# Kernel optimization log

Hardware: AMD Instinct MI355X
Metric: run time of the kernel (lower is better)

## Reference

```python
import jax, jax.numpy as jnp
import numpy as np

B, T, D, S = 32, 4096, 64, 64
H = 128  # emission MLP hidden width
EPS = 1e-10
NEG = 1e10


def setup_inputs() -> dict:
    key = jax.random.key(0)
    ks = jax.random.split(key, 8)

    def dense_init(k, shape):
        return jax.random.normal(k, shape, jnp.float32) / jnp.sqrt(shape[0])

    return {
        "observations": jax.random.normal(ks[0], (B, T, D), jnp.float32),
        "W1": dense_init(ks[1], (D, H)), "b1": jnp.zeros((H,), jnp.float32),
        "W2": dense_init(ks[2], (H, H)), "b2": jnp.zeros((H,), jnp.float32),
        "W3": dense_init(ks[3], (H, S)), "b3": jnp.zeros((S,), jnp.float32),
        "log_trans_matrix": jax.random.normal(ks[4], (S, S), jnp.float32) * 0.1,
        "log_init_probs": jnp.zeros((S,), jnp.float32),
        "log_r": jnp.ones((S,), jnp.float32),
        "logit_p": jnp.zeros((S,), jnp.float32),
    }


def reference(observations, W1, b1, W2, b2, W3, b3,
              log_trans_matrix, log_init_probs, log_r, logit_p):
    # ---- emission MLP + softmax ----  (B,T,D) -> (B,T,S)
    h = jax.nn.relu(observations @ W1 + b1)
    h = jax.nn.relu(h @ W2 + b2)
    emission_probs = jax.nn.softmax(h @ W3 + b3, axis=-1)
    log_em = jnp.log(emission_probs + EPS)  # (B,T,S)

    # ---- transition probs: self-transition masked softmax (S,S) ----
    eye = jnp.eye(S, dtype=jnp.float32)
    masked_logits = log_trans_matrix * (1.0 - eye) - NEG * eye
    trans_probs = jax.nn.softmax(masked_logits, axis=-1)  # (S,S)
    log_trans = jnp.log(trans_probs + EPS)

    # ---- forward recursion (scan over time) ----
    # NOTE: t=0 uses log(emission) WITHOUT eps, matching the torch source.
    la0 = jax.nn.log_softmax(log_init_probs) + jnp.log(emission_probs[:, 0])  # (B,S)

    def fstep(la, le_t):  # la:(B,S), le_t:(B,S)
        la_t = jax.nn.logsumexp(la[:, :, None] + log_trans[None], axis=1) + le_t
        return la_t, la_t

    le_rest = jnp.swapaxes(log_em[:, 1:], 0, 1)  # (T-1,B,S)
    _, las = jax.lax.scan(fstep, la0, le_rest)
    log_alpha = jnp.concatenate([la0[:, None], jnp.swapaxes(las, 0, 1)], axis=1)  # (B,T,S)

    # ---- backward recursion ----
    lbT = jnp.zeros((B, S), jnp.float32)

    def bstep(lb, le_t1):  # combine emission(t+1)+beta(t+1) over next-state axis
        lb_t = jax.nn.logsumexp(log_trans[None] + (le_t1 + lb)[:, None, :], axis=2)
        return lb_t, lb_t

    _, lbs = jax.lax.scan(bstep, lbT, le_rest[::-1])  # lbs[0] is t=T-2
    log_beta = jnp.concatenate(
        [jnp.swapaxes(lbs, 0, 1)[:, ::-1], lbT[:, None]], axis=1)  # (B,T,S)

    # ---- posteriors ----
    log_gamma = log_alpha + log_beta
    log_gamma = log_gamma - jax.nn.logsumexp(log_gamma, axis=-1, keepdims=True)
    state_probs = jnp.exp(log_gamma)  # (B,T,S)
    state_marginals = state_probs.mean(axis=1)  # (B,S)

    # ---- expected durations (negative binomial) for all states ----
    r = jnp.exp(log_r)
    p = jax.nn.sigmoid(logit_p)
    expected_durations = r * (1.0 - p) / p  # (S,)

    # log-likelihood from final forward messages
    log_likelihood = jax.nn.logsumexp(log_alpha[:, -1], axis=-1)  # (B,)

    return state_probs, state_marginals, expected_durations, log_likelihood
```

## Files before the change

kernel.cpp:

```cpp
#include <hip/hip_runtime.h>

#define B_ 32
#define T_ 4096
#define D_ 64
#define H_ 128
#define S_ 64
#define BTS (B_*T_*S_)

#define NCH 256
#define CL  16
#define WU  16

#define EM_OFF    0
#define ALPHA_OFF (BTS/2)
#define BETA_OFF  BTS
#define P_OFF     (2*BTS)
#define PT_OFF    (2*BTS + 4096)
#define INITP_OFF (2*BTS + 8192)
#define WSPLIT_OFF (2*BTS - 32768)
#define SP_OFF   0
#define MARG_OFF BTS
#define DUR_OFF  (BTS + 2048)
#define LL_OFF   (BTS + 2112)

typedef __attribute__((ext_vector_type(8))) short short8;
typedef __attribute__((ext_vector_type(4))) short short4v;
typedef __attribute__((ext_vector_type(4))) float f32x4;
#define MFMA_BF16 __builtin_amdgcn_mfma_f32_16x16x32_bf16

__device__ __forceinline__ float wsum(float v) {
    #pragma unroll
    for (int m = 1; m < 64; m <<= 1) v += __shfl_xor(v, m, 64);
    return v;
}
__device__ __forceinline__ float wmax(float v) {
    #pragma unroll
    for (int m = 1; m < 64; m <<= 1) v = fmaxf(v, __shfl_xor(v, m, 64));
    return v;
}
__device__ __forceinline__ unsigned short bfhi(float x) {
    return (unsigned short)(__float_as_uint(x) >> 16);
}
__device__ __forceinline__ float bf2f(unsigned short h) {
    return __uint_as_float(((unsigned int)h) << 16);
}
__device__ __forceinline__ short8 cvt8(const float* x8) {
    int hv[4];
    #pragma unroll
    for (int p = 0; p < 4; p++) {
        int h;
        asm("v_cvt_pk_bf16_f32 %0, %1, %2" : "=v"(h) : "v"(x8[2*p]), "v"(x8[2*p+1]));
        hv[p] = h;
    }
    return *(short8*)hv;
}
__device__ __forceinline__ unsigned short bf16r(float x) {
    int h;
    asm("v_cvt_pk_bf16_f32 %0, %1, %2" : "=v"(h) : "v"(x), "v"(x));
    return (unsigned short)h;
}

__global__ __launch_bounds__(256) void prep_k(const float* __restrict__ LT,
                                              const float* __restrict__ lip,
                                              const float* __restrict__ logr,
                                              const float* __restrict__ logitp,
                                              const float* __restrict__ W1,
                                              const float* __restrict__ W2,
                                              const float* __restrict__ W3,
                                              float* __restrict__ ws,
                                              float* __restrict__ out) {
    int tid = threadIdx.x, wid = tid >> 6, lane = tid & 63;
    if (blockIdx.x == 0) {
        for (int r = wid; r < S_; r += 4) {
            float x = (lane == r) ? -1e10f : LT[r * S_ + lane];
            float m = wmax(x);
            float e = __expf(x - m);
            float s = wsum(e);
            float p = e / s + 1e-10f;
            ws[P_OFF  + r * S_ + lane] = p;
            ws[PT_OFF + lane * S_ + r] = p;
        }
        if (wid == 0) {
            float x = lip[lane];
            float m = wmax(x);
            float e = __expf(x - m);
            float s = wsum(e);
            ws[INITP_OFF + lane] = e / s;
        } else if (wid == 1) {
            float r = __expf(logr[lane]);
            float p = 1.f / (1.f + __expf(-logitp[lane]));
            out[DUR_OFF + lane] = r * (1.f - p) / p;
        }
        for (int i = tid; i < B_ * S_; i += 256) out[MARG_OFF + i] = 0.f;
        if (tid < B_) out[LL_OFF + tid] = 0.f;
    }
    int gid = blockIdx.x * 256 + tid, gstr = gridDim.x * 256;
    unsigned short* wsp = (unsigned short*)(ws + WSPLIT_OFF);
    for (int i = gid; i < 8192; i += gstr) {
        int j = i >> 6, d = i & 63;
        wsp[i] = bfhi(W1[d * 128 + j]);
    }
    for (int i = gid; i < 16384; i += gstr) {
        int j = i >> 7, k = i & 127;
        wsp[16384 + i] = bfhi(W2[k * 128 + j]);
    }
    for (int i = gid; i < 8192; i += gstr) {
        int s = i >> 7, k = i & 127;
        wsp[49152 + i] = bfhi(W3[k * 64 + s]);
    }
}

__global__ __launch_bounds__(256) void mlp_k(const float* __restrict__ obs,
                                             const unsigned short* __restrict__ wsp,
                                             const float* __restrict__ b1,
                                             const float* __restrict__ b2,
                                             const float* __restrict__ b3,
                                             unsigned short* __restrict__ em) {
    __shared__ unsigned short hl[4 * 2 * 2176];
    int tid = threadIdx.x, wid = tid >> 6, lane = tid & 63;
    int c = lane & 15, q = lane >> 4;
    unsigned short* hb = hl + wid * 4352;
    int r0 = blockIdx.x * 128 + wid * 32;

    short8 a1[2][2];
    #pragma unroll
    for (int mt = 0; mt < 2; mt++) {
        #pragma unroll
        for (int kq = 0; kq < 2; kq++) {
            const float* xp = obs + (size_t)(r0 + mt * 16 + c) * 64 + kq * 32 + q * 8;
            float x8[8];
            *(float4*)x8       = *(const float4*)xp;
            *(float4*)(x8 + 4) = *(const float4*)(xp + 4);
            a1[mt][kq] = cvt8(x8);
        }
    }

    #pragma unroll
    for (int nt = 0; nt < 8; nt++) {
        const unsigned short* wp = wsp + (nt * 16 + c) * 64 + q * 8;
        short8 bh0 = *(const short8*)(wp);
        short8 bh1 = *(const short8*)(wp + 32);
        float bb = b1[nt * 16 + c];
        #pragma unroll
        for (int mt = 0; mt < 2; mt++) {
            f32x4 acc = {0.f, 0.f, 0.f, 0.f};
            acc = MFMA_BF16(a1[mt][0], bh0, acc, 0, 0, 0);
            acc = MFMA_BF16(a1[mt][1], bh1, acc, 0, 0, 0);
            #pragma unroll
            for (int r = 0; r < 4; r++)
                hb[mt * 2176 + (q * 4 + r) * 136 + nt * 16 + c] =
                    bf16r(fmaxf(acc[r] + bb, 0.f));
        }
    }

    short8 a2[2][4];
    #pragma unroll
    for (int mt = 0; mt < 2; mt++)
        #pragma unroll
        for (int kq = 0; kq < 4; kq++)
            a2[mt][kq] = *(const short8*)&hb[mt * 2176 + c * 136 + kq * 32 + q * 8];
    __asm__ __volatile__("s_waitcnt lgkmcnt(0)" ::: "memory");

    #pragma unroll
    for (int nt = 0; nt < 8; nt++) {
        const unsigned short* wp = wsp + 16384 + (nt * 16 + c) * 128 + q * 8;
        short8 bh[4];
        #pragma unroll
        for (int kq = 0; kq < 4; kq++)
            bh[kq] = *(const short8*)(wp + kq * 32);
        float bb = b2[nt * 16 + c];
        #pragma unroll
        for (int mt = 0; mt < 2; mt++) {
            f32x4 acc = {0.f, 0.f, 0.f, 0.f};
            #pragma unroll
            for (int kq = 0; kq < 4; kq++)
                acc = MFMA_BF16(a2[mt][kq], bh[kq], acc, 0, 0, 0);
            #pragma unroll
            for (int r = 0; r < 4; r++)
                hb[mt * 2176 + (q * 4 + r) * 136 + nt * 16 + c] =
                    bf16r(fmaxf(acc[r] + bb, 0.f));
        }
    }

    short8 a3[2][4];
    #pragma unroll
    for (int mt = 0; mt < 2; mt++)
        #pragma unroll
        for (int kq = 0; kq < 4; kq++)
            a3[mt][kq] = *(const short8*)&hb[mt * 2176 + c * 136 + kq * 32 + q * 8];
    __asm__ __volatile__("s_waitcnt lgkmcnt(0)" ::: "memory");

    f32x4 L[2][4];
    #pragma unroll
    for (int nt = 0; nt < 4; nt++) {
        const unsigned short* wp = wsp + 49152 + (nt * 16 + c) * 128 + q * 8;
        short8 bh[4];
        #pragma unroll
        for (int kq = 0; kq < 4; kq++)
            bh[kq] = *(const short8*)(wp + kq * 32);
        #pragma unroll
        for (int mt = 0; mt < 2; mt++) {
            f32x4 acc = {0.f, 0.f, 0.f, 0.f};
            #pragma unroll
            for (int kq = 0; kq < 4; kq++)
                acc = MFMA_BF16(a3[mt][kq], bh[kq], acc, 0, 0, 0);
            L[mt][nt] = acc;
        }
    }

    float bb3[4];
    #pragma unroll
    for (int nt = 0; nt < 4; nt++) bb3[nt] = b3[nt * 16 + c];
    #pragma unroll
    for (int mt = 0; mt < 2; mt++) {
        #pragma unroll
        for (int r = 0; r < 4; r++) {
            float v[4];
            #pragma unroll
            for (int nt = 0; nt < 4; nt++) v[nt] = L[mt][nt][r] + bb3[nt];
            float m = fmaxf(fmaxf(v[0], v[1]), fmaxf(v[2], v[3]));
            #pragma unroll
            for (int msk = 1; msk < 16; msk <<= 1) m = fmaxf(m, __shfl_xor(m, msk, 64));
            float e[4], s = 0.f;
            #pragma unroll
            for (int nt = 0; nt < 4; nt++) { e[nt] = __expf(v[nt] - m); s += e[nt]; }
            #pragma unroll
            for (int msk = 1; msk < 16; msk <<= 1) s += __shfl_xor(s, msk, 64);
            float rs = __builtin_amdgcn_rcpf(s);
            size_t row = (size_t)(r0 + mt * 16 + q * 4 + r);
            #pragma unroll
            for (int nt = 0; nt < 4; nt++)
                em[row * 64 + nt * 16 + c] = bf16r(e[nt] * rs);
        }
    }
}

__global__ __launch_bounds__(64) void scan_k(const unsigned short* __restrict__ em,
                                             const float* __restrict__ Pm,
                                             const float* __restrict__ PTm,
                                             const float* __restrict__ initp,
                                             unsigned short* __restrict__ alpha,
                                             unsigned short* __restrict__ beta,
                                             float* __restrict__ ll) {
    __shared__ float lds[16 * 68];
    const int lane = threadIdx.x, c = lane & 15, q = lane >> 4;
    int blk = blockIdx.x;
    const bool isf = blk < 2 * NCH;
    int lin = isf ? blk : blk - 2 * NCH;
    int bg = lin / NCH, ch = lin % NCH;
    const int b = bg * 16 + c;
    const float* M = isf ? PTm : Pm;

    short8 Bh[4][2];
    #pragma unroll
    for (int nt = 0; nt < 4; nt++) {
        #pragma unroll
        for (int kf = 0; kf < 2; kf++) {
            const float* mp = M + (nt * 16 + c) * 64 + kf * 32 + q * 8;
            float m8[8];
            *(float4*)m8       = *(const float4*)mp;
            *(float4*)(m8 + 4) = *(const float4*)(mp + 4);
            Bh[nt][kf] = cvt8(m8);
        }
    }

    const size_t ebase = (size_t)b * T_ * 64 + q * 8;
    unsigned short* outp = isf ? alpha : beta;
    const int wrofs = (q * 4) * 68 + c;
    const int rdofs = c * 68 + q * 8;

    float w[16];
    float rcpS, C = 0.f;

    auto loadE = [&](int t, float* e) {
        const unsigned short* p = em + ebase + (size_t)t * 64;
        short8 u0 = *(const short8*)(p);
        short8 u1 = *(const short8*)(p + 32);
        #pragma unroll
        for (int i = 0; i < 8; i++) {
            e[i]     = bf2f((unsigned short)u0[i]);
            e[8 + i] = bf2f((unsigned short)u1[i]);
        }
    };
    auto storeY = [&](const float* y, int t) {
        unsigned short* p = outp + ebase + (size_t)t * 64;
        *(short8*)(p)      = cvt8(y);
        *(short8*)(p + 32) = cvt8(y + 8);
    };
    auto chainsum = [&](const float* y) {
        float s = ((y[0]+y[1])+(y[2]+y[3])) + ((y[4]+y[5])+(y[6]+y[7]))
                + ((y[8]+y[9])+(y[10]+y[11])) + ((y[12]+y[13])+(y[14]+y[15]));
        s += __shfl_xor(s, 16, 64);
        s += __shfl_xor(s, 32, 64);
        return s;
    };
    auto matstep = [&](const float* z, float* y) {
        short8 ah0 = cvt8(z);
        short8 ah1 = cvt8(z + 8);
        f32x4 Dv[4];
        #pragma unroll
        for (int nt = 0; nt < 4; nt++) {
            f32x4 acc = {0.f, 0.f, 0.f, 0.f};
            acc = MFMA_BF16(ah0, Bh[nt][0], acc, 0, 0, 0);
            acc = MFMA_BF16(ah1, Bh[nt][1], acc, 0, 0, 0);
            Dv[nt] = acc;
        }
        #pragma unroll
        for (int r = 0; r < 4; r++) {
            lds[wrofs + r * 68]      = Dv[0][r];
            lds[wrofs + r * 68 + 16] = Dv[1][r];
            lds[wrofs + r * 68 + 32] = Dv[2][r];
            lds[wrofs + r * 68 + 48] = Dv[3][r];
        }
        __asm__ __volatile__("s_waitcnt lgkmcnt(0)" ::: "memory");
        *(float4*)(y)      = *(const float4*)&lds[rdofs];
        *(float4*)(y + 4)  = *(const float4*)&lds[rdofs + 4];
        *(float4*)(y + 8)  = *(const float4*)&lds[rdofs + 32];
        *(float4*)(y + 12) = *(const float4*)&lds[rdofs + 36];
        __asm__ __volatile__("s_waitcnt lgkmcnt(0)" ::: "memory");
    };

    if (isf) {
        const int wlo = ch * CL, te = wlo + CL - 1;
        int ts, nwarm;
        if (ch == 0) {
            float e[16], ip[16];
            loadE(0, e);
            const float* pp = initp + q * 8;
            *(float4*)(ip)      = *(const float4*)(pp);
            *(float4*)(ip + 4)  = *(const float4*)(pp + 4);
            *(float4*)(ip + 8)  = *(const float4*)(pp + 32);
            *(float4*)(ip + 12) = *(const float4*)(pp + 36);
            #pragma unroll
            for (int i = 0; i < 16; i++) w[i] = ip[i] * e[i];
            storeY(w, 0);
            float s = chainsum(w);
            rcpS = __builtin_amdgcn_rcpf(s);
            C = __log2f(s);
            ts = 1; nwarm = 0;
        } else {
            ts = wlo - WU; if (ts < 1) ts = 1;
            nwarm = wlo - ts;
            float e[16];
            loadE(ts - 1, e);
            #pragma unroll
            for (int i = 0; i < 16; i++) w[i] = e[i] + 1e-10f;
            float s = chainsum(w);
            rcpS = __builtin_amdgcn_rcpf(s);
            C = 0.f;
        }
        auto stepF = [&](int t, bool owned) {
            float e[16];
            loadE(t, e);
            float y[16];
            matstep(w, y);
            float epsr = 1e-10f * rcpS;
            #pragma unroll
            for (int i = 0; i < 16; i++) y[i] *= fmaf(e[i], rcpS, epsr);
            float s = chainsum(y);
            if (owned) { C += __log2f(s); storeY(y, t); }
            rcpS = __builtin_amdgcn_rcpf(s);
            #pragma unroll
            for (int i = 0; i < 16; i++) w[i] = y[i];
        };
        for (int i = 0; i < nwarm; i++) stepF(ts + i, false);
        for (int t = wlo > 0 ? wlo : 1; t <= te; t++) stepF(t, true);
        if (q == 0) atomicAdd(&ll[b], C * 0.69314718056f);
    } else {
        const int tlo = ch * CL;
        const int whi = (ch == NCH - 1) ? T_ - 2 : tlo + CL - 1;
        int ts, nwarm;
        if (ch == NCH - 1) {
            float ones[16];
            #pragma unroll
            for (int i = 0; i < 16; i++) ones[i] = 1.f;
            storeY(ones, T_ - 1);
            float e[16];
            loadE(T_ - 1, e);
            #pragma unroll
            for (int i = 0; i < 16; i++) w[i] = e[i] + 1e-10f;
            rcpS = 1.f / 64.f;
            nwarm = 0; ts = T_ - 2;
        } else {
            ts = whi + WU; if (ts > T_ - 2) ts = T_ - 2;
            nwarm = ts - whi;
            float e[16];
            loadE(ts + 1, e);
            #pragma unroll
            for (int i = 0; i < 16; i++) w[i] = e[i] + 1e-10f;
            rcpS = 1.f / 64.f;
        }
        auto stepB = [&](int t, bool owned) {
            float e[16];
            loadE(t, e);
            float y[16];
            matstep(w, y);
            #pragma unroll
            for (int i = 0; i < 16; i++) y[i] *= rcpS;
            float s = chainsum(y);
            if (owned) storeY(y, t);
            rcpS = __builtin_amdgcn_rcpf(s);
            #pragma unroll
            for (int i = 0; i < 16; i++) w[i] = y[i] * (e[i] + 1e-10f);
        };
        for (int i = 0; i < nwarm; i++) stepB(ts - i, false);
        for (int t = whi; t >= tlo; t--) stepB(t, true);
    }
}

__global__ __launch_bounds__(256) void gamma_k(const unsigned short* __restrict__ a16,
                                               const unsigned short* __restrict__ b16,
                                               float* __restrict__ out) {
    int tid = threadIdx.x;
    int wid = tid >> 6, lane = tid & 63;
    int c = lane & 15, q = lane >> 4;
    int b = blockIdx.x >> 5;
    int tile = blockIdx.x & 31;
    int t0 = tile * 128 + wid * 32;
    float m0 = 0.f, m1 = 0.f, m2 = 0.f, m3 = 0.f;
    #pragma unroll
    for (int it = 0; it < 8; it++) {
        int row = t0 + it * 4 + q;
        size_t off = ((size_t)b * T_ + row) * 64 + c * 4;
        short4v av = *(const short4v*)&a16[off];
        short4v bv = *(const short4v*)&b16[off];
        float px = bf2f((unsigned short)av[0]) * bf2f((unsigned short)bv[0]);
        float py = bf2f((unsigned short)av[1]) * bf2f((unsigned short)bv[1]);
        float pz = bf2f((unsigned short)av[2]) * bf2f((unsigned short)bv[2]);
        float pw = bf2f((unsigned short)av[3]) * bf2f((unsigned short)bv[3]);
        float s = (px + py) + (pz + pw);
        s += __shfl_xor(s, 1, 64);
        s += __shfl_xor(s, 2, 64);
        s += __shfl_xor(s, 4, 64);
        s += __shfl_xor(s, 8, 64);
        float rs = __builtin_amdgcn_rcpf(fmaxf(s, 1e-37f));
        float4 g;
        g.x = px * rs; g.y = py * rs; g.z = pz * rs; g.w = pw * rs;
        *(float4*)&out[SP_OFF + off] = g;
        m0 += g.x; m1 += g.y; m2 += g.z; m3 += g.w;
    }
    m0 += __shfl_xor(m0, 16, 64); m0 += __shfl_xor(m0, 32, 64);
    m1 += __shfl_xor(m1, 16, 64); m1 += __shfl_xor(m1, 32, 64);
    m2 += __shfl_xor(m2, 16, 64); m2 += __shfl_xor(m2, 32, 64);
    m3 += __shfl_xor(m3, 16, 64); m3 += __shfl_xor(m3, 32, 64);
    if (q == 0) {
        const float sc = 1.0f / T_;
        atomicAdd(&out[MARG_OFF + b * 64 + 4 * c + 0], m0 * sc);
        atomicAdd(&out[MARG_OFF + b * 64 + 4 * c + 1], m1 * sc);
        atomicAdd(&out[MARG_OFF + b * 64 + 4 * c + 2], m2 * sc);
        atomicAdd(&out[MARG_OFF + b * 64 + 4 * c + 3], m3 * sc);
    }
}

extern "C" void kernel_launch(void* const* d_in, const int* in_sizes, int n_in,
                              void* d_out, int out_size, void* d_ws, size_t ws_size,
                              hipStream_t stream) {
    (void)in_sizes; (void)n_in; (void)out_size; (void)ws_size;
    const float* obs    = (const float*)d_in[0];
    const float* W1     = (const float*)d_in[1];
    const float* b1     = (const float*)d_in[2];
    const float* W2     = (const float*)d_in[3];
    const float* b2     = (const float*)d_in[4];
    const float* W3     = (const float*)d_in[5];
    const float* b3     = (const float*)d_in[6];
    const float* LT     = (const float*)d_in[7];
    const float* lip    = (const float*)d_in[8];
    const float* logr   = (const float*)d_in[9];
    const float* logitp = (const float*)d_in[10];
    float* out = (float*)d_out;
    float* ws  = (float*)d_ws;

    unsigned short* em16 = (unsigned short*)(ws + EM_OFF);
    unsigned short* al16 = (unsigned short*)(ws + ALPHA_OFF);
    unsigned short* be16 = (unsigned short*)(ws + BETA_OFF);

    hipLaunchKernelGGL(prep_k, dim3(64), dim3(256), 0, stream,
                       LT, lip, logr, logitp, W1, W2, W3, ws, out);
    hipLaunchKernelGGL(mlp_k, dim3(1024), dim3(256), 0, stream,
                       obs, (const unsigned short*)(ws + WSPLIT_OFF),
                       b1, b2, b3, em16);
    hipLaunchKernelGGL(scan_k, dim3(4 * NCH), dim3(64), 0, stream,
                       em16, ws + P_OFF, ws + PT_OFF, ws + INITP_OFF,
                       al16, be16, out + LL_OFF);
    hipLaunchKernelGGL(gamma_k, dim3(1024), dim3(256), 0, stream,
                       al16, be16, out);
}
```

Measured before the change: 200.4 us.

## Prefetch next MLP weight tile during MFMAs and reduce WU to 12

The three emission MLP layers now software-pipeline their weight loads. The next column tile of weights is loaded into registers while the MFMAs for the current tile run, so global/L2 load latency is hidden behind compute. Separately, the WU constant (a warm-up length in the chunked recursion) drops from 16 to 12, which cuts redundant work in the scan but may affect accuracy at chunk boundaries. The prefetch raises register pressure.

```diff
diff --git a/kernel.cpp b/kernel.cpp
--- a/kernel.cpp
+++ b/kernel.cpp
@@ -9,7 +9,7 @@
 
 #define NCH 256
 #define CL  16
-#define WU  16
+#define WU  12
 
 #define EM_OFF    0
 #define ALPHA_OFF (BTS/2)
@@ -135,21 +135,29 @@
         }
     }
 
-    #pragma unroll
-    for (int nt = 0; nt < 8; nt++) {
-        const unsigned short* wp = wsp + (nt * 16 + c) * 64 + q * 8;
-        short8 bh0 = *(const short8*)(wp);
-        short8 bh1 = *(const short8*)(wp + 32);
-        float bb = b1[nt * 16 + c];
-        #pragma unroll
-        for (int mt = 0; mt < 2; mt++) {
-            f32x4 acc = {0.f, 0.f, 0.f, 0.f};
-            acc = MFMA_BF16(a1[mt][0], bh0, acc, 0, 0, 0);
-            acc = MFMA_BF16(a1[mt][1], bh1, acc, 0, 0, 0);
-            #pragma unroll
-            for (int r = 0; r < 4; r++)
-                hb[mt * 2176 + (q * 4 + r) * 136 + nt * 16 + c] =
-                    bf16r(fmaxf(acc[r] + bb, 0.f));
+    {
+        short8 wa = *(const short8*)(wsp + (0 * 16 + c) * 64 + q * 8);
+        short8 wb = *(const short8*)(wsp + (0 * 16 + c) * 64 + q * 8 + 32);
+        #pragma unroll
+        for (int nt = 0; nt < 8; nt++) {
+            short8 na, nb;
+            if (nt < 7) {
+                const unsigned short* np = wsp + ((nt + 1) * 16 + c) * 64 + q * 8;
+                na = *(const short8*)(np);
+                nb = *(const short8*)(np + 32);
+            }
+            float bb = b1[nt * 16 + c];
+            #pragma unroll
+            for (int mt = 0; mt < 2; mt++) {
+                f32x4 acc = {0.f, 0.f, 0.f, 0.f};
+                acc = MFMA_BF16(a1[mt][0], wa, acc, 0, 0, 0);
+                acc = MFMA_BF16(a1[mt][1], wb, acc, 0, 0, 0);
+                #pragma unroll
+                for (int r = 0; r < 4; r++)
+                    hb[mt * 2176 + (q * 4 + r) * 136 + nt * 16 + c] =
+                        bf16r(fmaxf(acc[r] + bb, 0.f));
+            }
+            if (nt < 7) { wa = na; wb = nb; }
         }
     }
 
@@ -161,24 +169,35 @@
             a2[mt][kq] = *(const short8*)&hb[mt * 2176 + c * 136 + kq * 32 + q * 8];
     __asm__ __volatile__("s_waitcnt lgkmcnt(0)" ::: "memory");
 
-    #pragma unroll
-    for (int nt = 0; nt < 8; nt++) {
-        const unsigned short* wp = wsp + 16384 + (nt * 16 + c) * 128 + q * 8;
-        short8 bh[4];
+    {
+        short8 bh[4], bn[4];
         #pragma unroll
         for (int kq = 0; kq < 4; kq++)
-            bh[kq] = *(const short8*)(wp + kq * 32);
-        float bb = b2[nt * 16 + c];
-        #pragma unroll
-        for (int mt = 0; mt < 2; mt++) {
-            f32x4 acc = {0.f, 0.f, 0.f, 0.f};
-            #pragma unroll
-            for (int kq = 0; kq < 4; kq++)
-                acc = MFMA_BF16(a2[mt][kq], bh[kq], acc, 0, 0, 0);
-            #pragma unroll
-            for (int r = 0; r < 4; r++)
-                hb[mt * 2176 + (q * 4 + r) * 136 + nt * 16 + c] =
-                    bf16r(fmaxf(acc[r] + bb, 0.f));
+            bh[kq] = *(const short8*)(wsp + 16384 + (0 * 16 + c) * 128 + kq * 32 + q * 8);
+        #pragma unroll
+        for (int nt = 0; nt < 8; nt++) {
+            if (nt < 7) {
+                const unsigned short* np = wsp + 16384 + ((nt + 1) * 16 + c) * 128 + q * 8;
+                #pragma unroll
+                for (int kq = 0; kq < 4; kq++)
+                    bn[kq] = *(const short8*)(np + kq * 32);
+            }
+            float bb = b2[nt * 16 + c];
+            #pragma unroll
+            for (int mt = 0; mt < 2; mt++) {
+                f32x4 acc = {0.f, 0.f, 0.f, 0.f};
+                #pragma unroll
+                for (int kq = 0; kq < 4; kq++)
+                    acc = MFMA_BF16(a2[mt][kq], bh[kq], acc, 0, 0, 0);
+                #pragma unroll
+                for (int r = 0; r < 4; r++)
+                    hb[mt * 2176 + (q * 4 + r) * 136 + nt * 16 + c] =
+                        bf16r(fmaxf(acc[r] + bb, 0.f));
+            }
+            if (nt < 7) {
+                #pragma unroll
+                for (int kq = 0; kq < 4; kq++) bh[kq] = bn[kq];
+            }
         }
     }
 
@@ -191,20 +210,31 @@
     __asm__ __volatile__("s_waitcnt lgkmcnt(0)" ::: "memory");
 
     f32x4 L[2][4];
-    #pragma unroll
-    for (int nt = 0; nt < 4; nt++) {
-        const unsigned short* wp = wsp + 49152 + (nt * 16 + c) * 128 + q * 8;
-        short8 bh[4];
+    {
+        short8 bh[4], bn[4];
         #pragma unroll
         for (int kq = 0; kq < 4; kq++)
-            bh[kq] = *(const short8*)(wp + kq * 32);
-        #pragma unroll
-        for (int mt = 0; mt < 2; mt++) {
-            f32x4 acc = {0.f, 0.f, 0.f, 0.f};
-            #pragma unroll
-            for (int kq = 0; kq < 4; kq++)
-                acc = MFMA_BF16(a3[mt][kq], bh[kq], acc, 0, 0, 0);
-            L[mt][nt] = acc;
+            bh[kq] = *(const short8*)(wsp + 49152 + (0 * 16 + c) * 128 + kq * 32 + q * 8);
+        #pragma unroll
+        for (int nt = 0; nt < 4; nt++) {
+            if (nt < 3) {
+                const unsigned short* np = wsp + 49152 + ((nt + 1) * 16 + c) * 128 + q * 8;
+                #pragma unroll
+                for (int kq = 0; kq < 4; kq++)
+                    bn[kq] = *(const short8*)(np + kq * 32);
+            }
+            #pragma unroll
+            for (int mt = 0; mt < 2; mt++) {
+                f32x4 acc = {0.f, 0.f, 0.f, 0.f};
+                #pragma unroll
+                for (int kq = 0; kq < 4; kq++)
+                    acc = MFMA_BF16(a3[mt][kq], bh[kq], acc, 0, 0, 0);
+                L[mt][nt] = acc;
+            }
+            if (nt < 3) {
+                #pragma unroll
+                for (int kq = 0; kq < 4; kq++) bh[kq] = bn[kq];
+            }
         }
     }
 
```

Result: no change. 199.6 us (-0.4%).
